# Optimization experiments

Measured on AMD Instinct MI355X. Metric: run time of the kernel, lower is better.

## Reference

```python
import jax, jax.numpy as jnp
import numpy as np

HIDDEN = 4096
N_HEADS = 32
N_KV_HEADS = 8
HEAD_DIM = HIDDEN // N_HEADS  # 128
Q_SIZE = N_HEADS * HEAD_DIM
KV_SIZE = N_KV_HEADS * HEAD_DIM
ROPE_THETA = 10000.0
EPS = 1e-5
SCALE = HEAD_DIM ** -0.5


def _headwise_layernorm(x, weight, eps):
    # x: [B,S,H,D], weight: [H,D]; LayerNorm over last dim (head_dim), fp32 math
    xf = x.astype(jnp.float32)
    mean = xf.mean(-1, keepdims=True)
    var = jnp.square(xf - mean).mean(-1, keepdims=True)
    y = (xf - mean) * jax.lax.rsqrt(var + eps)
    return (weight.astype(jnp.float32) * y).astype(x.dtype)


def _rope_gptj(x, positions):
    # non-neox (GPT-J) style: rotate interleaved pairs. x: [B,S,H,D]
    half = HEAD_DIM // 2
    inv_freq = 1.0 / (ROPE_THETA ** (jnp.arange(0, HEAD_DIM, 2, dtype=jnp.float32) / HEAD_DIM))
    ang = positions.astype(jnp.float32)[..., None] * inv_freq  # [B,S,half]
    cos = jnp.cos(ang)[:, :, None, :]  # [B,S,1,half]
    sin = jnp.sin(ang)[:, :, None, :]
    x1 = x[..., 0::2]
    x2 = x[..., 1::2]
    o1 = x1 * cos - x2 * sin
    o2 = x2 * cos + x1 * sin
    # re-interleave
    out = jnp.stack([o1, o2], axis=-1).reshape(x.shape)
    return out.astype(x.dtype)


def setup_inputs() -> dict:
    key = jax.random.key(0)
    k1, k2, k3, k4 = jax.random.split(key, 4)
    B, S = 2, 2048
    positions = jnp.tile(jnp.arange(S, dtype=jnp.int32)[None, :], (B, 1))
    hidden_states = jax.random.normal(k1, (B, S, HIDDEN), dtype=jnp.float32)
    Wqkv = jax.random.normal(k2, (HIDDEN, Q_SIZE + 2 * KV_SIZE), dtype=jnp.float32) * (HIDDEN ** -0.5)
    Wo = jax.random.normal(k3, (Q_SIZE, HIDDEN), dtype=jnp.float32) * (Q_SIZE ** -0.5)
    kq, kk = jax.random.split(k4)
    q_norm_w = jnp.ones((N_HEADS, HEAD_DIM), jnp.float32) + 0.02 * jax.random.normal(kq, (N_HEADS, HEAD_DIM))
    k_norm_w = jnp.ones((N_KV_HEADS, HEAD_DIM), jnp.float32) + 0.02 * jax.random.normal(kk, (N_KV_HEADS, HEAD_DIM))
    return {"positions": positions, "hidden_states": hidden_states, "Wqkv": Wqkv,
            "q_norm_w": q_norm_w, "k_norm_w": k_norm_w, "Wo": Wo}


def reference(positions, hidden_states, Wqkv, q_norm_w, k_norm_w, Wo):
    B, S, _ = hidden_states.shape
    qkv = hidden_states @ Wqkv  # [B,S,Q+2KV]
    q, k, v = jnp.split(qkv, [Q_SIZE, Q_SIZE + KV_SIZE], axis=-1)
    q = q.reshape(B, S, N_HEADS, HEAD_DIM)
    k = k.reshape(B, S, N_KV_HEADS, HEAD_DIM)
    v = v.reshape(B, S, N_KV_HEADS, HEAD_DIM)
    # per-head qk-norm
    q = _headwise_layernorm(q, q_norm_w, EPS)
    k = _headwise_layernorm(k, k_norm_w, EPS)
    # non-neox RoPE
    q = _rope_gptj(q, positions)
    k = _rope_gptj(k, positions)
    # GQA: repeat kv heads
    n_rep = N_HEADS // N_KV_HEADS
    k = jnp.repeat(k, n_rep, axis=2)  # [B,S,H,D]
    v = jnp.repeat(v, n_rep, axis=2)
    scores = jnp.einsum('bqhd,bkhd->bhqk', q, k) * SCALE
    causal = jnp.tril(jnp.ones((S, S), dtype=bool))
    scores = jnp.where(causal[None, None], scores, jnp.finfo(scores.dtype).min)
    probs = jax.nn.softmax(scores, axis=-1)
    attn = jnp.einsum('bhqk,bkhd->bqhd', probs, v).reshape(B, S, Q_SIZE)
    return attn @ Wo
```

## Files before the change

### kernel.cpp

```cpp
#include <hip/hip_runtime.h>
#include <hip/hip_bf16.h>
#include <cstdint>

typedef unsigned short u16;
typedef unsigned int u32;
typedef __attribute__((ext_vector_type(8))) short bf16x8;
typedef __attribute__((ext_vector_type(4))) float f32x4;
typedef __attribute__((ext_vector_type(16))) float f32x16;
typedef __attribute__((ext_vector_type(4))) unsigned int u32x4;

#define HIDDEN 4096
#define NH 32
#define NKV 8
#define HD 128
#define QSZ 4096
#define KVSZ 1024
#define QKV_N 6144
#define SEQ 2048
#define NB 2
#define NTOK (NB*SEQ)
#define ATT_SCALE 0.08838834764831845f
#define LOG2E 1.4426950408889634f
#define LN_EPS 1e-5f
#define THRD 12.0f

__device__ __forceinline__ u16 f2bf(float f) {
  union { float f; u32 u; } a; a.f = f;
  u32 r = a.u + 0x7fffu + ((a.u >> 16) & 1u);
  return (u16)(r >> 16);
}
__device__ __forceinline__ float bf2f(u16 h) {
  union { u32 u; float f; } a; a.u = ((u32)h) << 16;
  return a.f;
}

__device__ __forceinline__ void gload_lds16(const void* g, void* l) {
  __builtin_amdgcn_global_load_lds(
      (const __attribute__((address_space(1))) void*)g,
      (__attribute__((address_space(3))) void*)l,
      16, 0, 0);
}

__global__ __launch_bounds__(256)
void conv_f32_bf16(const float* __restrict__ in, u16* __restrict__ out, int n8) {
  int i = blockIdx.x * 256 + threadIdx.x;
  if (i >= n8) return;
  const float4* p = (const float4*)in + (size_t)i * 2;
  float4 v0 = p[0], v1 = p[1];
  u32x4 o;
  o.x = (u32)f2bf(v0.x) | ((u32)f2bf(v0.y) << 16);
  o.y = (u32)f2bf(v0.z) | ((u32)f2bf(v0.w) << 16);
  o.z = (u32)f2bf(v1.x) | ((u32)f2bf(v1.y) << 16);
  o.w = (u32)f2bf(v1.z) | ((u32)f2bf(v1.w) << 16);
  ((u32x4*)out)[i] = o;
}

__global__ __launch_bounds__(256)
void transp_f32_bf16(const float* __restrict__ in, u16* __restrict__ out, int R, int C) {
  __shared__ float tile[32][33];
  int c0 = blockIdx.x << 5, r0 = blockIdx.y << 5;
  int tx = threadIdx.x & 31, ty = threadIdx.x >> 5;
  #pragma unroll
  for (int j = 0; j < 32; j += 8)
    tile[ty + j][tx] = in[(long)(r0 + ty + j) * C + c0 + tx];
  __syncthreads();
  #pragma unroll
  for (int j = 0; j < 32; j += 8)
    out[(long)(c0 + ty + j) * R + r0 + tx] = f2bf(tile[tx][ty + j]);
}

template<typename OutT>
__global__ __launch_bounds__(512, 2)
void gemm_bt5(const u16* __restrict__ A, const u16* __restrict__ Bt,
              OutT* __restrict__ C, int N, int K) {
  extern __shared__ char smem[];
  const int t = threadIdx.x;
  const int lane = t & 63, w = t >> 6;
  const int wr = w >> 2, wc = w & 3;
  const int l31 = lane & 31, g2 = lane >> 5;
  const int bm = blockIdx.y, bn = blockIdx.x;

  const u16* pA[4]; const u16* pB[4];
  int dS[4];
  #pragma unroll
  for (int i = 0; i < 4; ++i) {
    int ci = t + i * 512;
    int row = ci >> 3;
    int c = (ci & 7) ^ (row & 7);
    pA[i] = A  + (long)(bm * 256 + row) * K + (c << 3);
    pB[i] = Bt + (long)(bn * 256 + row) * K + (c << 3);
    dS[i] = (i * 512 + w * 64) * 16;
  }

  const int arowB = (wr * 128 + l31) * 128;
  const int browB = 32768 + (wc * 64 + l31) * 128;

  f32x16 acc[4][2];
  #pragma unroll
  for (int i = 0; i < 4; ++i)
    #pragma unroll
    for (int j = 0; j < 2; ++j)
      #pragma unroll
      for (int r = 0; r < 16; ++r) acc[i][j][r] = 0.f;

  const int nt = K >> 6;
  char* cb = smem;
  char* sb = smem + 65536;

  #pragma unroll
  for (int i = 0; i < 4; ++i) gload_lds16(pA[i], cb + dS[i]);
  #pragma unroll
  for (int i = 0; i < 4; ++i) gload_lds16(pB[i], cb + 32768 + dS[i]);
  asm volatile("s_waitcnt vmcnt(0)" ::: "memory");
  __builtin_amdgcn_s_barrier();
  __builtin_amdgcn_sched_barrier(0);

  #define READ_KK(dst, kkv) { \
    const int pcb = ((((kkv) * 2 + g2)) ^ (l31 & 7)) << 4; \
    dst[0] = *(const bf16x8*)(cb + arowB + pcb); \
    dst[1] = *(const bf16x8*)(cb + arowB + 4096 + pcb); \
    dst[2] = *(const bf16x8*)(cb + arowB + 8192 + pcb); \
    dst[3] = *(const bf16x8*)(cb + arowB + 12288 + pcb); \
    dst[4] = *(const bf16x8*)(cb + browB + pcb); \
    dst[5] = *(const bf16x8*)(cb + browB + 4096 + pcb); }
  #define MFMA_KK(f) { \
    __builtin_amdgcn_s_setprio(1); \
    acc[0][0] = __builtin_amdgcn_mfma_f32_32x32x16_bf16(f[0], f[4], acc[0][0], 0, 0, 0); \
    acc[0][1] = __builtin_amdgcn_mfma_f32_32x32x16_bf16(f[0], f[5], acc[0][1], 0, 0, 0); \
    acc[1][0] = __builtin_amdgcn_mfma_f32_32x32x16_bf16(f[1], f[4], acc[1][0], 0, 0, 0); \
    acc[1][1] = __builtin_amdgcn_mfma_f32_32x32x16_bf16(f[1], f[5], acc[1][1], 0, 0, 0); \
    acc[2][0] = __builtin_amdgcn_mfma_f32_32x32x16_bf16(f[2], f[4], acc[2][0], 0, 0, 0); \
    acc[2][1] = __builtin_amdgcn_mfma_f32_32x32x16_bf16(f[2], f[5], acc[2][1], 0, 0, 0); \
    acc[3][0] = __builtin_amdgcn_mfma_f32_32x32x16_bf16(f[3], f[4], acc[3][0], 0, 0, 0); \
    acc[3][1] = __builtin_amdgcn_mfma_f32_32x32x16_bf16(f[3], f[5], acc[3][1], 0, 0, 0); \
    __builtin_amdgcn_s_setprio(0); }

  for (int tt = 0; tt < nt; ++tt) {
    const long sk = (long)((tt + 1 < nt) ? (tt + 1) : (nt - 1)) * 64;
    gload_lds16(pA[0] + sk, sb + dS[0]);
    gload_lds16(pA[1] + sk, sb + dS[1]);
    gload_lds16(pA[2] + sk, sb + dS[2]);
    gload_lds16(pA[3] + sk, sb + dS[3]);
    gload_lds16(pB[0] + sk, sb + 32768 + dS[0]);
    gload_lds16(pB[1] + sk, sb + 32768 + dS[1]);
    gload_lds16(pB[2] + sk, sb + 32768 + dS[2]);
    gload_lds16(pB[3] + sk, sb + 32768 + dS[3]);
    bf16x8 f0[6], f1[6];
    READ_KK(f0, 0);
    READ_KK(f1, 1);
    MFMA_KK(f0);
    READ_KK(f0, 2);
    MFMA_KK(f1);
    READ_KK(f1, 3);
    MFMA_KK(f0);
    MFMA_KK(f1);
    asm volatile("s_waitcnt vmcnt(0)" ::: "memory");
    __builtin_amdgcn_s_barrier();
    __builtin_amdgcn_sched_barrier(0);
    char* tmp = cb; cb = sb; sb = tmp;
  }
  #undef READ_KK
  #undef MFMA_KK

  #pragma unroll
  for (int mf = 0; mf < 4; ++mf)
    #pragma unroll
    for (int nf = 0; nf < 2; ++nf)
      #pragma unroll
      for (int r = 0; r < 16; ++r) {
        long row = bm * 256 + wr * 128 + mf * 32 + (r & 3) + 8 * (r >> 2) + 4 * g2;
        long col = bn * 256 + wc * 64 + nf * 32 + l31;
        float v = acc[mf][nf][r];
        if constexpr (sizeof(OutT) == 2) C[row * N + col] = f2bf(v);
        else                             C[row * N + col] = v;
      }
}

__device__ __forceinline__ void ln_rope_head(const u16* __restrict__ src,
                                             const float* __restrict__ wgt,
                                             u16* __restrict__ dst,
                                             int lane, float sa, float ca, float scale) {
  u32 xr = *(const u32*)(src + 2 * lane);
  float x1 = bf2f((u16)(xr & 0xffffu)), x2 = bf2f((u16)(xr >> 16));
  float ssum = x1 + x2;
  #pragma unroll
  for (int off = 1; off < 64; off <<= 1) ssum += __shfl_xor(ssum, off);
  float mean = ssum * (1.0f / 128.0f);
  float e1 = x1 - mean, e2 = x2 - mean;
  float vv = e1 * e1 + e2 * e2;
  #pragma unroll
  for (int off = 1; off < 64; off <<= 1) vv += __shfl_xor(vv, off);
  float rstd = rsqrtf(vv * (1.0f / 128.0f) + LN_EPS);
  float y1 = e1 * rstd * wgt[2 * lane];
  float y2 = e2 * rstd * wgt[2 * lane + 1];
  float o1 = (y1 * ca - y2 * sa) * scale;
  float o2 = (y2 * ca + y1 * sa) * scale;
  *(u32*)(dst + 2 * lane) = (u32)f2bf(o1) | ((u32)f2bf(o2) << 16);
}

__global__ __launch_bounds__(512)
void ln_rope(const u16* __restrict__ qkv, const int* __restrict__ pos,
             const float* __restrict__ qw, const float* __restrict__ kw,
             u16* __restrict__ qo, u16* __restrict__ ko) {
  const int s = blockIdx.x, b = blockIdx.y;
  const int t = threadIdx.x, lane = t & 63, w = t >> 6;
  const long base = (long)(b * SEQ + s) * QKV_N;
  const int p = pos[b * SEQ + s];
  const float expo = (float)(2 * lane) * (1.0f / 128.0f);
  const float inv_freq = exp2f(-expo * 13.287712379549449f);
  float sa, ca;
  sincosf((float)p * inv_freq, &sa, &ca);
  #pragma unroll
  for (int hh = 0; hh < 4; ++hh) {
    int h = w + hh * 8;
    ln_rope_head(qkv + base + h * HD, qw + h * HD,
                 qo + (((long)b * NH + h) * SEQ + s) * HD, lane, sa, ca,
                 ATT_SCALE * LOG2E);
  }
  ln_rope_head(qkv + base + QSZ + w * HD, kw + w * HD,
               ko + (((long)b * NKV + w) * SEQ + s) * HD, lane, sa, ca, 1.0f);
}

__global__ __launch_bounds__(256)
void v_transp(const u16* __restrict__ qkv, u16* __restrict__ vt) {
  __shared__ u16 tile[32][33];
  int s0 = blockIdx.x * 32, d0 = blockIdx.y * 32;
  int bk = blockIdx.z;
  int b = bk >> 3, kvh = bk & 7;
  int tx = threadIdx.x & 31, ty = threadIdx.x >> 5;
  const u16* src = qkv + ((long)(b * SEQ) + s0) * QKV_N + QSZ + KVSZ + kvh * HD + d0;
  #pragma unroll
  for (int j = 0; j < 32; j += 8)
    tile[ty + j][tx] = src[(long)(ty + j) * QKV_N + tx];
  __syncthreads();
  u16* dst = vt + (((long)bk) * HD + d0) * SEQ + s0;
  #pragma unroll
  for (int j = 0; j < 32; j += 8)
    dst[(long)(ty + j) * SEQ + tx] = tile[tx][ty + j];
}

__global__ __launch_bounds__(512, 2)
void flash_attn2(const u16* __restrict__ Qg, const u16* __restrict__ Kg,
                 const u16* __restrict__ Vtg, u16* __restrict__ Og) {
  const int lin = blockIdx.x;
  const int b = lin >> 8;
  const int rem = lin & 255;
  const int h = rem >> 3;
  const int q3 = rem & 7;
  const int qt = b ? (7 - q3) : q3;
  const int kvh = h >> 2;
  const int t = threadIdx.x, lane = t & 63, w = t >> 6;
  const int hh = lane >> 5, l31 = lane & 31;
  const int wq0 = qt * 256 + w * 32;
  const int q = wq0 + l31;

  __shared__ u16 Klds[2][64 * 128];
  __shared__ u16 Vlds[2][128 * 64];

  const u16* Qbase = Qg + (((long)b * NH + h) * SEQ + q) * HD + hh * 8;
  bf16x8 qf[8];
  #pragma unroll
  for (int ks = 0; ks < 8; ++ks) qf[ks] = *(const bf16x8*)(Qbase + ks * 16);

  f32x16 o[4];
  #pragma unroll
  for (int i = 0; i < 4; ++i)
    #pragma unroll
    for (int r = 0; r < 16; ++r) o[i][r] = 0.f;
  float m = -1e30f, l = 0.f;

  const u16* Kbase = Kg + ((long)b * NKV + kvh) * (long)SEQ * HD;
  const u16* Vtbase = Vtg + ((long)b * NKV + kvh) * (long)HD * SEQ;
  const int nt = qt * 4 + 4;

  auto STAGE = [&](int buf, int kt) {
    const int kv0 = kt * 64;
    #pragma unroll
    for (int i = 0; i < 2; ++i) {
      int c = t + i * 512;
      int kv = c >> 4, cc = c & 15;
      int cl = (cc & 8) | ((cc ^ kv) & 7);
      gload_lds16(Kbase + (long)(kv0 + kv) * HD + cl * 8,
                  (char*)(&Klds[buf][0]) + (i * 512 + w * 64) * 16);
    }
    #pragma unroll
    for (int i = 0; i < 2; ++i) {
      int c = t + i * 512;
      int d = c >> 3, cc = c & 7;
      int cl = cc ^ (d & 7);
      gload_lds16(Vtbase + (long)d * SEQ + kv0 + cl * 8,
                  (char*)(&Vlds[buf][0]) + (i * 512 + w * 64) * 16);
    }
  };

  STAGE(0, 0);
  __syncthreads();
  int cur = 0;
  for (int kt = 0; kt < nt; ++kt) {
    const int kv0 = kt * 64;
    if (kt + 1 < nt) STAGE(cur ^ 1, kt + 1);
    if (kv0 <= wq0 + 31) {
      const char* Kb = (const char*)(&Klds[cur][0]);
      const char* Vb = (const char*)(&Vlds[cur][0]);
      f32x16 st[2];
      #pragma unroll
      for (int tt = 0; tt < 2; ++tt)
        #pragma unroll
        for (int r = 0; r < 16; ++r) st[tt][r] = 0.f;
      __builtin_amdgcn_s_setprio(1);
      #pragma unroll
      for (int tt = 0; tt < 2; ++tt) {
        if (kv0 + tt * 32 <= wq0 + 31) {
          #pragma unroll
          for (int ks = 0; ks < 8; ++ks) {
            int ch = ks * 2 + hh;
            int pc = (ch & 8) | ((ch ^ l31) & 7);
            bf16x8 kf = *(const bf16x8*)(Kb + (tt * 32 + l31) * 256 + pc * 16);
            st[tt] = __builtin_amdgcn_mfma_f32_32x32x16_bf16(kf, qf[ks], st[tt], 0, 0, 0);
          }
        }
      }
      __builtin_amdgcn_s_setprio(0);
      if (kv0 + 63 > wq0) {
        #pragma unroll
        for (int tt = 0; tt < 2; ++tt)
          #pragma unroll
          for (int r = 0; r < 16; ++r) {
            int kva = kv0 + tt * 32 + (r & 3) + 8 * (r >> 2) + 4 * hh;
            if (kva > q) st[tt][r] = -1e30f;
          }
      }
      float p0 = -1e30f, p1 = -1e30f, p2 = -1e30f, p3 = -1e30f;
      #pragma unroll
      for (int tt = 0; tt < 2; ++tt)
        #pragma unroll
        for (int r = 0; r < 16; r += 4) {
          p0 = fmaxf(p0, st[tt][r]);
          p1 = fmaxf(p1, st[tt][r + 1]);
          p2 = fmaxf(p2, st[tt][r + 2]);
          p3 = fmaxf(p3, st[tt][r + 3]);
        }
      float mx = fmaxf(fmaxf(p0, p1), fmaxf(p2, p3));
      mx = fmaxf(mx, __shfl_xor(mx, 32));
      if (!__all(mx - m <= THRD)) {
        float mn = fmaxf(m, mx);
        float sc = exp2f(m - mn);
        m = mn;
        float scr[16];
        #pragma unroll
        for (int r = 0; r < 16; ++r)
          scr[r] = __shfl(sc, (r & 3) + 8 * (r >> 2) + 4 * hh);
        #pragma unroll
        for (int db = 0; db < 4; ++db)
          #pragma unroll
          for (int r = 0; r < 16; ++r) o[db][r] *= scr[r];
        l *= sc;
      }
      float s0 = 0.f, s1 = 0.f, s2 = 0.f, s3 = 0.f;
      #pragma unroll
      for (int tt = 0; tt < 2; ++tt)
        #pragma unroll
        for (int r = 0; r < 16; r += 4) {
          float e0 = exp2f(st[tt][r] - m);
          float e1 = exp2f(st[tt][r + 1] - m);
          float e2 = exp2f(st[tt][r + 2] - m);
          float e3 = exp2f(st[tt][r + 3] - m);
          st[tt][r] = e0; st[tt][r + 1] = e1; st[tt][r + 2] = e2; st[tt][r + 3] = e3;
          s0 += e0; s1 += e1; s2 += e2; s3 += e3;
        }
      float rs = (s0 + s1) + (s2 + s3);
      rs += __shfl_xor(rs, 32);
      l += rs;
      bf16x8 pa[4];
      #pragma unroll
      for (int k4 = 0; k4 < 4; ++k4) {
        int s8 = (k4 & 1) * 8, tt = k4 >> 1;
        u32 x0 = (u32)f2bf(st[tt][s8 + 0]) | ((u32)f2bf(st[tt][s8 + 1]) << 16);
        u32 x1 = (u32)f2bf(st[tt][s8 + 2]) | ((u32)f2bf(st[tt][s8 + 3]) << 16);
        u32 y0 = (u32)f2bf(st[tt][s8 + 4]) | ((u32)f2bf(st[tt][s8 + 5]) << 16);
        u32 y1 = (u32)f2bf(st[tt][s8 + 6]) | ((u32)f2bf(st[tt][s8 + 7]) << 16);
        u32 x0s = (u32)__shfl_xor((int)x0, 32), x1s = (u32)__shfl_xor((int)x1, 32);
        u32 y0s = (u32)__shfl_xor((int)y0, 32), y1s = (u32)__shfl_xor((int)y1, 32);
        union { u32 u[4]; bf16x8 v; } pk;
        pk.u[0] = hh ? y0s : x0;
        pk.u[1] = hh ? y1s : x1;
        pk.u[2] = hh ? y0 : x0s;
        pk.u[3] = hh ? y1 : x1s;
        pa[k4] = pk.v;
      }
      __builtin_amdgcn_s_setprio(1);
      #pragma unroll
      for (int k4 = 0; k4 < 4; ++k4)
        #pragma unroll
        for (int db = 0; db < 4; ++db) {
          int ch = k4 * 2 + hh;
          int pcc = ch ^ (l31 & 7);
          bf16x8 vf = *(const bf16x8*)(Vb + (db * 32 + l31) * 128 + pcc * 16);
          o[db] = __builtin_amdgcn_mfma_f32_32x32x16_bf16(pa[k4], vf, o[db], 0, 0, 0);
        }
      __builtin_amdgcn_s_setprio(0);
    }
    __syncthreads();
    cur ^= 1;
  }
  float linv = 1.0f / l;
  float li[16];
  #pragma unroll
  for (int r = 0; r < 16; ++r)
    li[r] = __shfl(linv, (r & 3) + 8 * (r >> 2) + 4 * hh);
  #pragma unroll
  for (int db = 0; db < 4; ++db)
    #pragma unroll
    for (int r = 0; r < 16; ++r) {
      int qr = wq0 + (r & 3) + 8 * (r >> 2) + 4 * hh;
      Og[((long)b * SEQ + qr) * QSZ + h * HD + db * 32 + l31] = f2bf(o[db][r] * li[r]);
    }
}

extern "C" void kernel_launch(void* const* d_in, const int* in_sizes, int n_in,
                              void* d_out, int out_size, void* d_ws, size_t ws_size,
                              hipStream_t stream) {
  const int*   positions = (const int*)d_in[0];
  const float* hidden    = (const float*)d_in[1];
  const float* Wqkv      = (const float*)d_in[2];
  const float* qnw       = (const float*)d_in[3];
  const float* knw       = (const float*)d_in[4];
  const float* Wo        = (const float*)d_in[5];
  float* out = (float*)d_out;
  char* ws = (char*)d_ws;
  const size_t MB = 1024 * 1024;
  u16* hbf   = (u16*)(ws + 0);
  u16* WqkvT = (u16*)(ws + 32 * MB);
  u16* qkvb  = (u16*)(ws + 80 * MB);
  u16* q_arr = (u16*)(ws + 0);
  u16* k_arr = (u16*)(ws + 32 * MB);
  u16* vt_arr= (u16*)(ws + 40 * MB);
  u16* WoT   = (u16*)(ws + 48 * MB);
  u16* Oarr  = (u16*)(ws + 80 * MB);

  const int GEMM_LDS = 2 * 65536;
  (void)hipFuncSetAttribute((const void*)&gemm_bt5<u16>,
        hipFuncAttributeMaxDynamicSharedMemorySize, GEMM_LDS);
  (void)hipFuncSetAttribute((const void*)&gemm_bt5<float>,
        hipFuncAttributeMaxDynamicSharedMemorySize, GEMM_LDS);

  conv_f32_bf16<<<dim3(NTOK * HIDDEN / 8 / 256), 256, 0, stream>>>(hidden, hbf, NTOK * HIDDEN / 8);
  transp_f32_bf16<<<dim3(QKV_N / 32, HIDDEN / 32), 256, 0, stream>>>(Wqkv, WqkvT, HIDDEN, QKV_N);
  gemm_bt5<u16><<<dim3(QKV_N / 256, NTOK / 256), 512, GEMM_LDS, stream>>>(hbf, WqkvT, qkvb, QKV_N, HIDDEN);
  ln_rope<<<dim3(SEQ, NB), 512, 0, stream>>>(qkvb, positions, qnw, knw, q_arr, k_arr);
  v_transp<<<dim3(SEQ / 32, HD / 32, NB * NKV), 256, 0, stream>>>(qkvb, vt_arr);
  transp_f32_bf16<<<dim3(HIDDEN / 32, QSZ / 32), 256, 0, stream>>>(Wo, WoT, QSZ, HIDDEN);
  flash_attn2<<<dim3(512), 512, 0, stream>>>(q_arr, k_arr, vt_arr, Oarr);
  gemm_bt5<float><<<dim3(HIDDEN / 256, NTOK / 256), 512, GEMM_LDS, stream>>>(Oarr, WoT, out, HIDDEN, QSZ);
}
```

Before: 589.7 us.

## Triple-buffer A tiles in the GEMM to prefetch two k-steps ahead

The bf16 GEMM now keeps three LDS buffers for A tiles and two for B tiles. A loads are issued two k-iterations ahead and B loads one ahead. The per-iteration wait becomes vmcnt(4) instead of a full drain, so the newest A loads can stay in flight across the barrier. This is meant to hide global-to-LDS latency better in both the QKV and output projections, at the cost of raising dynamic LDS use to 160KB per block.

```diff
diff --git a/kernel.cpp b/kernel.cpp
--- a/kernel.cpp
+++ b/kernel.cpp
@@ -71,7 +71,7 @@
 
 template<typename OutT>
 __global__ __launch_bounds__(512, 2)
-void gemm_bt5(const u16* __restrict__ A, const u16* __restrict__ Bt,
+void gemm_bt8(const u16* __restrict__ A, const u16* __restrict__ Bt,
               OutT* __restrict__ C, int N, int K) {
   extern __shared__ char smem[];
   const int t = threadIdx.x;
@@ -93,7 +93,7 @@
   }
 
   const int arowB = (wr * 128 + l31) * 128;
-  const int browB = 32768 + (wc * 64 + l31) * 128;
+  const int browB = (wc * 64 + l31) * 128;
 
   f32x16 acc[4][2];
   #pragma unroll
@@ -104,25 +104,33 @@
       for (int r = 0; r < 16; ++r) acc[i][j][r] = 0.f;
 
   const int nt = K >> 6;
-  char* cb = smem;
-  char* sb = smem + 65536;
-
-  #pragma unroll
-  for (int i = 0; i < 4; ++i) gload_lds16(pA[i], cb + dS[i]);
-  #pragma unroll
-  for (int i = 0; i < 4; ++i) gload_lds16(pB[i], cb + 32768 + dS[i]);
-  asm volatile("s_waitcnt vmcnt(0)" ::: "memory");
+
+  #define STAGE_A(dst, koff) { \
+    gload_lds16(pA[0] + (koff), (dst) + dS[0]); \
+    gload_lds16(pA[1] + (koff), (dst) + dS[1]); \
+    gload_lds16(pA[2] + (koff), (dst) + dS[2]); \
+    gload_lds16(pA[3] + (koff), (dst) + dS[3]); }
+  #define STAGE_B(dst, koff) { \
+    gload_lds16(pB[0] + (koff), (dst) + dS[0]); \
+    gload_lds16(pB[1] + (koff), (dst) + dS[1]); \
+    gload_lds16(pB[2] + (koff), (dst) + dS[2]); \
+    gload_lds16(pB[3] + (koff), (dst) + dS[3]); }
+
+  STAGE_B(smem + 98304, 0);
+  STAGE_A(smem, 0);
+  STAGE_A(smem + 32768, 64);
+  asm volatile("s_waitcnt vmcnt(4)" ::: "memory");
   __builtin_amdgcn_s_barrier();
   __builtin_amdgcn_sched_barrier(0);
 
-  #define READ_KK(dst, kkv) { \
-    const int pcb = ((((kkv) * 2 + g2)) ^ (l31 & 7)) << 4; \
-    dst[0] = *(const bf16x8*)(cb + arowB + pcb); \
-    dst[1] = *(const bf16x8*)(cb + arowB + 4096 + pcb); \
-    dst[2] = *(const bf16x8*)(cb + arowB + 8192 + pcb); \
-    dst[3] = *(const bf16x8*)(cb + arowB + 12288 + pcb); \
-    dst[4] = *(const bf16x8*)(cb + browB + pcb); \
-    dst[5] = *(const bf16x8*)(cb + browB + 4096 + pcb); }
+  #define READ_KK(dst, kkv, cbA, cbB) { \
+    const int pcb = (((kkv) * 2 + g2) ^ (l31 & 7)) << 4; \
+    dst[0] = *(const bf16x8*)((cbA) + arowB + pcb); \
+    dst[1] = *(const bf16x8*)((cbA) + arowB + 4096 + pcb); \
+    dst[2] = *(const bf16x8*)((cbA) + arowB + 8192 + pcb); \
+    dst[3] = *(const bf16x8*)((cbA) + arowB + 12288 + pcb); \
+    dst[4] = *(const bf16x8*)((cbB) + browB + pcb); \
+    dst[5] = *(const bf16x8*)((cbB) + browB + 4096 + pcb); }
   #define MFMA_KK(f) { \
     __builtin_amdgcn_s_setprio(1); \
     acc[0][0] = __builtin_amdgcn_mfma_f32_32x32x16_bf16(f[0], f[4], acc[0][0], 0, 0, 0); \
@@ -135,32 +143,35 @@
     acc[3][1] = __builtin_amdgcn_mfma_f32_32x32x16_bf16(f[3], f[5], acc[3][1], 0, 0, 0); \
     __builtin_amdgcn_s_setprio(0); }
 
+  int ia = 0;
   for (int tt = 0; tt < nt; ++tt) {
-    const long sk = (long)((tt + 1 < nt) ? (tt + 1) : (nt - 1)) * 64;
-    gload_lds16(pA[0] + sk, sb + dS[0]);
-    gload_lds16(pA[1] + sk, sb + dS[1]);
-    gload_lds16(pA[2] + sk, sb + dS[2]);
-    gload_lds16(pA[3] + sk, sb + dS[3]);
-    gload_lds16(pB[0] + sk, sb + 32768 + dS[0]);
-    gload_lds16(pB[1] + sk, sb + 32768 + dS[1]);
-    gload_lds16(pB[2] + sk, sb + 32768 + dS[2]);
-    gload_lds16(pB[3] + sk, sb + 32768 + dS[3]);
+    const char* cbA = smem + ia * 32768;
+    const char* cbB = smem + 98304 + (tt & 1) * 32768;
+    const long skB = (long)((tt + 1 < nt) ? (tt + 1) : (nt - 1)) * 64;
+    char* sbB = smem + 98304 + ((tt + 1) & 1) * 32768;
+    STAGE_B(sbB, skB);
+    const long skA = (long)((tt + 2 < nt) ? (tt + 2) : (nt - 1)) * 64;
+    int ia2 = ia + 2; if (ia2 >= 3) ia2 -= 3;
+    char* sbA = smem + ia2 * 32768;
+    STAGE_A(sbA, skA);
     bf16x8 f0[6], f1[6];
-    READ_KK(f0, 0);
-    READ_KK(f1, 1);
+    READ_KK(f0, 0, cbA, cbB);
+    READ_KK(f1, 1, cbA, cbB);
     MFMA_KK(f0);
-    READ_KK(f0, 2);
+    READ_KK(f0, 2, cbA, cbB);
     MFMA_KK(f1);
-    READ_KK(f1, 3);
+    READ_KK(f1, 3, cbA, cbB);
     MFMA_KK(f0);
     MFMA_KK(f1);
-    asm volatile("s_waitcnt vmcnt(0)" ::: "memory");
+    asm volatile("s_waitcnt vmcnt(4)" ::: "memory");
     __builtin_amdgcn_s_barrier();
     __builtin_amdgcn_sched_barrier(0);
-    char* tmp = cb; cb = sb; sb = tmp;
+    ++ia; if (ia >= 3) ia -= 3;
   }
   #undef READ_KK
   #undef MFMA_KK
+  #undef STAGE_A
+  #undef STAGE_B
 
   #pragma unroll
   for (int mf = 0; mf < 4; ++mf)
@@ -438,18 +449,18 @@
   u16* WoT   = (u16*)(ws + 48 * MB);
   u16* Oarr  = (u16*)(ws + 80 * MB);
 
-  const int GEMM_LDS = 2 * 65536;
-  (void)hipFuncSetAttribute((const void*)&gemm_bt5<u16>,
+  const int GEMM_LDS = 163840;
+  (void)hipFuncSetAttribute((const void*)&gemm_bt8<u16>,
         hipFuncAttributeMaxDynamicSharedMemorySize, GEMM_LDS);
-  (void)hipFuncSetAttribute((const void*)&gemm_bt5<float>,
+  (void)hipFuncSetAttribute((const void*)&gemm_bt8<float>,
         hipFuncAttributeMaxDynamicSharedMemorySize, GEMM_LDS);
 
   conv_f32_bf16<<<dim3(NTOK * HIDDEN / 8 / 256), 256, 0, stream>>>(hidden, hbf, NTOK * HIDDEN / 8);
   transp_f32_bf16<<<dim3(QKV_N / 32, HIDDEN / 32), 256, 0, stream>>>(Wqkv, WqkvT, HIDDEN, QKV_N);
-  gemm_bt5<u16><<<dim3(QKV_N / 256, NTOK / 256), 512, GEMM_LDS, stream>>>(hbf, WqkvT, qkvb, QKV_N, HIDDEN);
+  gemm_bt8<u16><<<dim3(QKV_N / 256, NTOK / 256), 512, GEMM_LDS, stream>>>(hbf, WqkvT, qkvb, QKV_N, HIDDEN);
   ln_rope<<<dim3(SEQ, NB), 512, 0, stream>>>(qkvb, positions, qnw, knw, q_arr, k_arr);
   v_transp<<<dim3(SEQ / 32, HD / 32, NB * NKV), 256, 0, stream>>>(qkvb, vt_arr);
   transp_f32_bf16<<<dim3(HIDDEN / 32, QSZ / 32), 256, 0, stream>>>(Wo, WoT, QSZ, HIDDEN);
   flash_attn2<<<dim3(512), 512, 0, stream>>>(q_arr, k_arr, vt_arr, Oarr);
-  gemm_bt5<float><<<dim3(HIDDEN / 256, NTOK / 256), 512, GEMM_LDS, stream>>>(Oarr, WoT, out, HIDDEN, QSZ);
-}
+  gemm_bt8<float><<<dim3(HIDDEN / 256, NTOK / 256), 512, GEMM_LDS, stream>>>(Oarr, WoT, out, HIDDEN, QSZ);
+}
```

New measurement: 593.9 us. About the same (+0.7%).
